# Kernel optimization log

Hardware: AMD Instinct MI355X
Metric: run time of the kernel (lower is better)

The kernel has to match this reference:

```python
import jax, jax.numpy as jnp
import numpy as np

# Master-Slave MoE: dense shared 'master' expert Mlp applied to every token,
# plus num_experts 'slave' Mlp experts combined via top-k softmax gating,
# output = master(x) + sum_k gate_k * expert_k(x). Each Mlp: fc2(gelu(fc1(x))).

DIM = 512
HID = 4 * DIM
NUM_EXPERTS = 8
TOP_K = 2


def mlp(x, w1, b1, w2, b2):
    h = jax.nn.gelu(jnp.einsum('bnd,dh->bnh', x, w1) + b1)
    return jnp.einsum('bnh,hd->bnd', h, w2) + b2


def setup_inputs() -> dict:
    key = jax.random.key(0)
    ks = jax.random.split(key, 10)
    B, N = 4, 4096
    s1 = 1.0 / np.sqrt(DIM)
    s2 = 1.0 / np.sqrt(HID)
    return {
        'x': jax.random.normal(ks[0], (B, N, DIM), jnp.float32),
        'gate_w': jax.random.normal(ks[1], (DIM, NUM_EXPERTS), jnp.float32) * s1,
        'master_w1': jax.random.normal(ks[2], (DIM, HID), jnp.float32) * s1,
        'master_b1': jnp.zeros((HID,), jnp.float32),
        'master_w2': jax.random.normal(ks[3], (HID, DIM), jnp.float32) * s2,
        'master_b2': jnp.zeros((DIM,), jnp.float32),
        'expert_w1': jax.random.normal(ks[4], (NUM_EXPERTS, DIM, HID), jnp.float32) * s1,
        'expert_b1': jnp.zeros((NUM_EXPERTS, HID), jnp.float32),
        'expert_w2': jax.random.normal(ks[5], (NUM_EXPERTS, HID, DIM), jnp.float32) * s2,
        'expert_b2': jnp.zeros((NUM_EXPERTS, DIM), jnp.float32),
    }


def reference(x, gate_w, master_w1, master_b1, master_w2, master_b2,
              expert_w1, expert_b1, expert_w2, expert_b2):
    B, N, D = x.shape
    # Router: top-k softmax gating over experts
    logits = jnp.einsum('bnd,de->bne', x, gate_w)  # [B,N,E]
    topv, topi = jax.lax.top_k(logits, TOP_K)       # [B,N,K]
    gates_k = jax.nn.softmax(topv, axis=-1)         # [B,N,K]
    # dense gate matrix [B,N,E] (zeros for non-selected experts)
    gates = jnp.zeros_like(logits)
    gates = jnp.take_along_axis(gates, topi, axis=-1)  # noop to keep shape clarity
    gates = jnp.zeros_like(logits).at[
        jnp.arange(B)[:, None, None],
        jnp.arange(N)[None, :, None],
        topi].set(gates_k)

    # Master (shared) expert applied to all tokens
    master_out = mlp(x, master_w1, master_b1, master_w2, master_b2)

    # Slave experts: compute per-expert Mlp (vectorized over experts),
    # combine with gate weights. Gate is sparse (only top-k nonzero),
    # mathematically equal to token routing.
    h = jax.nn.gelu(jnp.einsum('bnd,edh->ebnh', x, expert_w1)
                    + expert_b1[:, None, None, :])          # [E,B,N,H]
    eo = jnp.einsum('ebnh,ehd->ebnd', h, expert_w2) \
         + expert_b2[:, None, None, :]                       # [E,B,N,D]
    slave_out = jnp.einsum('bne,ebnd->bnd', gates, eo)

    return master_out + slave_out
```

## Files before the change

### kernel.cpp

```cpp
#include <hip/hip_runtime.h>

#define DIM 512
#define HID 2048
#define NE 8

typedef _Float16 half8v __attribute__((ext_vector_type(8)));
typedef _Float16 half4v __attribute__((ext_vector_type(4)));
typedef float f32x4 __attribute__((ext_vector_type(4)));

__device__ __forceinline__ void gload16(const void* g, void* l) {
  __builtin_amdgcn_global_load_lds(
      (const __attribute__((address_space(1))) void*)g,
      (__attribute__((address_space(3))) void*)l, 16, 0, 0);
}

__global__ void k_transpose_cast9(const float* __restrict__ src_e,
                                  const float* __restrict__ src_m,
                                  _Float16* __restrict__ dst, int R, int C) {
  __shared__ _Float16 ts[64][66];
  int z = blockIdx.z;
  const float* src = (z == NE) ? src_m : src_e + (size_t)z * R * C;
  _Float16* d = dst + (size_t)z * R * C;
  int c0 = blockIdx.x * 64, r0 = blockIdx.y * 64;
  int t = threadIdx.x;
  int rr = t >> 4, cc = (t & 15) * 4;
  #pragma unroll
  for (int i = 0; i < 4; i++) {
    int row = rr + i * 16;
    float4 v = *(const float4*)&src[(size_t)(r0 + row) * C + c0 + cc];
    ts[row][cc + 0] = (_Float16)v.x; ts[row][cc + 1] = (_Float16)v.y;
    ts[row][cc + 2] = (_Float16)v.z; ts[row][cc + 3] = (_Float16)v.w;
  }
  __syncthreads();
  int cr = t >> 4, rb = (t & 15) * 4;
  #pragma unroll
  for (int i = 0; i < 4; i++) {
    int c = cr + i * 16;
    half4v o = { ts[rb + 0][c], ts[rb + 1][c], ts[rb + 2][c], ts[rb + 3][c] };
    *(half4v*)&d[(size_t)(c0 + c) * R + r0 + rb] = o;
  }
}

#define RT_TOK 16
__global__ void k_router(const float* __restrict__ x, const float* __restrict__ gw,
                         _Float16* __restrict__ xb,
                         int* __restrict__ counts, int* __restrict__ perm,
                         float* __restrict__ pgate, int T) {
  __shared__ float xs[RT_TOK][520];
  __shared__ float gwt[8][520];
  __shared__ float lg[RT_TOK][8];
  int t = threadIdx.x;
  int tk0 = blockIdx.x * RT_TOK;
  for (int i = t; i < DIM * NE; i += 128) {
    int k = i >> 3, e = i & 7;
    gwt[e][k] = gw[i];
  }
  for (int i = t; i < RT_TOK * (DIM / 4); i += 128) {
    int row = i >> 7; int c4 = i & 127;
    float4 v = *(const float4*)&x[(size_t)(tk0 + row) * DIM + c4 * 4];
    xs[row][c4 * 4 + 0] = v.x; xs[row][c4 * 4 + 1] = v.y;
    xs[row][c4 * 4 + 2] = v.z; xs[row][c4 * 4 + 3] = v.w;
    half4v h = { (_Float16)v.x, (_Float16)v.y, (_Float16)v.z, (_Float16)v.w };
    *(half4v*)&xb[(size_t)(tk0 + row) * DIM + c4 * 4] = h;
  }
  __syncthreads();
  int tok = t >> 3, e = t & 7;
  float acc = 0.f;
  for (int k = 0; k < DIM; k += 4) {
    float4 xv = *(const float4*)&xs[tok][k];
    float4 wv = *(const float4*)&gwt[e][k];
    acc += xv.x * wv.x + xv.y * wv.y + xv.z * wv.z + xv.w * wv.w;
  }
  lg[tok][e] = acc;
  __syncthreads();
  if (t < RT_TOK) {
    float v0 = -1e30f, v1 = -1e30f; int i0 = 0, i1 = 0;
    #pragma unroll
    for (int j = 0; j < 8; j++) { float v = lg[t][j]; if (v > v0) { v0 = v; i0 = j; } }
    #pragma unroll
    for (int j = 0; j < 8; j++) { if (j == i0) continue; float v = lg[t][j]; if (v > v1) { v1 = v; i1 = j; } }
    float g0 = 1.f / (1.f + __expf(v1 - v0));
    float g1 = 1.f - g0;
    int token = tk0 + t;
    int p0 = atomicAdd(&counts[i0], 1);
    perm[i0 * T + p0] = token; pgate[i0 * T + p0] = g0;
    int p1 = atomicAdd(&counts[i1], 1);
    perm[i1 * T + p1] = token; pgate[i1 * T + p1] = g1;
  }
}


template<int K, int MODE>
__global__ __launch_bounds__(512, 1) void k_gemm(
    const _Float16* __restrict__ A,
    const _Float16* __restrict__ Bt,
    const float* __restrict__ ebias,
    const float* __restrict__ mbias,
    const int* __restrict__ counts,
    const int* __restrict__ perm,
    const float* __restrict__ pgate,
    _Float16* __restrict__ hout,
    float* __restrict__ out,
    int T) {
  constexpr int N = (MODE == 0) ? HID : DIM;
  constexpr int KT = K / 64;
  extern __shared__ char S[];
  int e = blockIdx.z;
  bool isM = (e == NE);
  int count = isM ? T : counts[e];
  int m0 = blockIdx.x * 256;
  if (m0 >= count) return;
  int n0 = blockIdx.y * 256;
  int hbase = 0;
  if (isM) hbase = 2 * T;
  else for (int i = 0; i < e; i++) hbase += counts[i];
  const _Float16* Be = Bt + (size_t)e * N * K;
  const float* be = isM ? mbias : ebias + (size_t)e * N;

  int t = threadIdx.x;
  int lane = t & 63;
  int wid = t >> 6;
  int wm = (wid >> 2) * 128;
  int wn = (wid & 3) * 64;

  int srow = t >> 3;
  int schunk = (t & 7) ^ (srow & 7);
  const char *aP0, *aP1, *aP2, *aP3, *bP0, *bP1, *bP2, *bP3;
  {
    int r0 = srow, r1 = 64 + srow, r2 = 128 + srow, r3 = 192 + srow;
    int p0 = m0 + r0; p0 = p0 < count ? p0 : count - 1;
    int p1 = m0 + r1; p1 = p1 < count ? p1 : count - 1;
    int p2 = m0 + r2; p2 = p2 < count ? p2 : count - 1;
    int p3 = m0 + r3; p3 = p3 < count ? p3 : count - 1;
    int a0, a1, a2, a3;
    if (MODE == 0) {
      a0 = isM ? p0 : perm[e * T + p0];
      a1 = isM ? p1 : perm[e * T + p1];
      a2 = isM ? p2 : perm[e * T + p2];
      a3 = isM ? p3 : perm[e * T + p3];
    } else {
      a0 = hbase + p0; a1 = hbase + p1; a2 = hbase + p2; a3 = hbase + p3;
    }
    aP0 = (const char*)(A + (size_t)a0 * K) + schunk * 16;
    aP1 = (const char*)(A + (size_t)a1 * K) + schunk * 16;
    aP2 = (const char*)(A + (size_t)a2 * K) + schunk * 16;
    aP3 = (const char*)(A + (size_t)a3 * K) + schunk * 16;
    bP0 = (const char*)(Be + (size_t)(n0 + r0) * K) + schunk * 16;
    bP1 = (const char*)(Be + (size_t)(n0 + r1) * K) + schunk * 16;
    bP2 = (const char*)(Be + (size_t)(n0 + r2) * K) + schunk * 16;
    bP3 = (const char*)(Be + (size_t)(n0 + r3) * K) + schunk * 16;
  }

  int l15 = lane & 15, l4 = lane >> 4, l7 = lane & 7;
  int roff0 = l15 * 128 + ((l4 ^ l7) << 4);
  int roff1 = l15 * 128 + (((4 + l4) ^ l7) << 4);

  f32x4 acc[8][4] = {};

  char* buf0 = S;
  char* buf1 = S + 65536;

#define STAGE(base, ktile) do { \
    const int off_ = (ktile) * 128; \
    gload16(aP0 + off_, (base) + t * 16); \
    gload16(aP1 + off_, (base) + 8192 + t * 16); \
    gload16(aP2 + off_, (base) + 16384 + t * 16); \
    gload16(aP3 + off_, (base) + 24576 + t * 16); \
    gload16(bP0 + off_, (base) + 32768 + t * 16); \
    gload16(bP1 + off_, (base) + 40960 + t * 16); \
    gload16(bP2 + off_, (base) + 49152 + t * 16); \
    gload16(bP3 + off_, (base) + 57344 + t * 16); \
  } while (0)

  STAGE(buf0, 0);
  for (int kt = 0; kt < KT; ++kt) {
    __builtin_amdgcn_s_barrier();
    if (kt + 1 < KT) {
      STAGE((kt & 1) ? buf0 : buf1, kt + 1);
      asm volatile("s_waitcnt vmcnt(8)" ::: "memory");
    } else {
      asm volatile("s_waitcnt vmcnt(0)" ::: "memory");
    }
    __builtin_amdgcn_sched_barrier(0);
    __builtin_amdgcn_s_barrier();
    const char* base = (kt & 1) ? buf1 : buf0;
    const char* ab = base;
    const char* bb = base + 32768;
    __builtin_amdgcn_s_setprio(1);
    #pragma unroll
    for (int kk = 0; kk < 2; ++kk) {
      int ro = kk ? roff1 : roff0;
      half8v af[8], bf[4];
      #pragma unroll
      for (int mi = 0; mi < 8; mi++)
        af[mi] = *(const half8v*)(ab + (wm + mi * 16) * 128 + ro);
      #pragma unroll
      for (int ni = 0; ni < 4; ni++)
        bf[ni] = *(const half8v*)(bb + (wn + ni * 16) * 128 + ro);
      #pragma unroll
      for (int mi = 0; mi < 8; mi++)
        #pragma unroll
        for (int ni = 0; ni < 4; ni++)
          acc[mi][ni] = __builtin_amdgcn_mfma_f32_16x16x32_f16(af[mi], bf[ni], acc[mi][ni], 0, 0, 0);
    }
    __builtin_amdgcn_s_setprio(0);
  }
#undef STAGE

  int cl = l15, rh = l4 * 4;
  float bv[4];
  #pragma unroll
  for (int ni = 0; ni < 4; ni++) bv[ni] = be[n0 + wn + ni * 16 + cl];
  #pragma unroll
  for (int mi = 0; mi < 8; mi++) {
    #pragma unroll
    for (int r = 0; r < 4; r++) {
      int pos = m0 + wm + mi * 16 + rh + r;
      if (pos >= count) continue;
      int orow; float g = 1.f;
      if (MODE == 0) orow = hbase + pos;
      else {
        orow = isM ? pos : perm[e * T + pos];
        if (!isM) g = pgate[e * T + pos];
      }
      #pragma unroll
      for (int ni = 0; ni < 4; ni++) {
        float v = acc[mi][ni][r] + bv[ni];
        int col = n0 + wn + ni * 16 + cl;
        if (MODE == 0) {
          float ge = v / (1.f + __expf(-1.5957691216057308f * (v + 0.044715f * v * v * v)));
          hout[(size_t)orow * HID + col] = (_Float16)ge;
        } else {
          unsafeAtomicAdd(&out[(size_t)orow * DIM + col], g * v);
        }
      }
    }
  }
}

extern "C" void kernel_launch(void* const* d_in, const int* in_sizes, int n_in,
                              void* d_out, int out_size, void* d_ws, size_t ws_size,
                              hipStream_t stream) {
  const float* x         = (const float*)d_in[0];
  const float* gate_w    = (const float*)d_in[1];
  const float* master_w1 = (const float*)d_in[2];
  const float* master_b1 = (const float*)d_in[3];
  const float* master_w2 = (const float*)d_in[4];
  const float* master_b2 = (const float*)d_in[5];
  const float* expert_w1 = (const float*)d_in[6];
  const float* expert_b1 = (const float*)d_in[7];
  const float* expert_w2 = (const float*)d_in[8];
  const float* expert_b2 = (const float*)d_in[9];
  float* out = (float*)d_out;
  int T = in_sizes[0] / DIM;

  char* p = (char*)d_ws;
  _Float16* xb   = (_Float16*)p; p += (size_t)T * DIM * 2;
  _Float16* wb1t = (_Float16*)p; p += (size_t)9 * HID * DIM * 2;
  _Float16* wb2t = (_Float16*)p; p += (size_t)9 * DIM * HID * 2;
  int*   counts  = (int*)p;      p += 256;
  int*   perm    = (int*)p;      p += (size_t)8 * T * 4;
  float* pgate   = (float*)p;    p += (size_t)8 * T * 4;
  _Float16* hbuf = (_Float16*)p; p += (size_t)3 * T * HID * 2;

  (void)hipFuncSetAttribute((const void*)&k_gemm<DIM, 0>,
                            hipFuncAttributeMaxDynamicSharedMemorySize, 131072);
  (void)hipFuncSetAttribute((const void*)&k_gemm<HID, 2>,
                            hipFuncAttributeMaxDynamicSharedMemorySize, 131072);

  hipMemsetAsync(counts, 0, 64, stream);
  hipMemsetAsync(out, 0, (size_t)T * DIM * 4, stream);

  k_router<<<T / RT_TOK, 128, 0, stream>>>(x, gate_w, xb, counts, perm, pgate, T);

  k_transpose_cast9<<<dim3(HID / 64, DIM / 64, 9), 256, 0, stream>>>(
      expert_w1, master_w1, wb1t, DIM, HID);
  k_transpose_cast9<<<dim3(DIM / 64, HID / 64, 9), 256, 0, stream>>>(
      expert_w2, master_w2, wb2t, HID, DIM);

  k_gemm<DIM, 0><<<dim3(T / 256, HID / 256, 9), 512, 131072, stream>>>(
      xb, wb1t, expert_b1, master_b1, counts, perm, nullptr,
      hbuf, nullptr, T);
  k_gemm<HID, 2><<<dim3(T / 256, DIM / 256, 9), 512, 131072, stream>>>(
      hbuf, wb2t, expert_b2, master_b2, counts, perm, pgate,
      nullptr, out, T);
}
```

Baseline: 717.3 us.

## Pack expert segments into a compact 1D grid and split master down-projection out

```diff
diff --git a/kernel.cpp b/kernel.cpp
--- a/kernel.cpp
+++ b/kernel.cpp
@@ -101,21 +101,43 @@
     const float* __restrict__ pgate,
     _Float16* __restrict__ hout,
     float* __restrict__ out,
-    int T) {
+    int T, int gxd8) {
   constexpr int N = (MODE == 0) ? HID : DIM;
   constexpr int KT = K / 64;
   extern __shared__ char S[];
-  int e = blockIdx.z;
-  bool isM = (e == NE);
-  int count = isM ? T : counts[e];
-  int m0 = blockIdx.x * 256;
-  if (m0 >= count) return;
+
+  int bxi = blockIdx.x;
+  bxi = (bxi & 7) * gxd8 + (bxi >> 3);
+  int bx = bxi * 256;
+  int e = 8, segbase = 0, count;
+  if (MODE == 1) {
+    #pragma unroll
+    for (int i = 0; i < 8; i++) segbase += (counts[i] + 255) & ~255;
+    count = T;
+  } else {
+    #pragma unroll
+    for (int i = 0; i < 8; i++) {
+      int seglen = (counts[i] + 255) & ~255;
+      if (e == 8 && bx < segbase + seglen) { e = i; break; }
+      segbase += seglen;
+    }
+    if (e == 8) {
+      if (MODE == 2) return;
+      count = T;
+      if (bx - segbase >= T) return;
+    } else {
+      count = counts[e];
+    }
+  }
+  bool isM = (e == 8);
+  int m0 = (MODE == 1) ? bx : bx - segbase;
+  if (MODE == 1 && m0 >= T) return;
   int n0 = blockIdx.y * 256;
-  int hbase = 0;
-  if (isM) hbase = 2 * T;
-  else for (int i = 0; i < e; i++) hbase += counts[i];
-  const _Float16* Be = Bt + (size_t)e * N * K;
-  const float* be = isM ? mbias : ebias + (size_t)e * N;
+  const _Float16* Be = Bt + (size_t)(MODE == 1 ? 8 : e) * N * K;
+  const float* be;
+  if (MODE == 0) be = isM ? mbias : ebias + (size_t)e * N;
+  else if (MODE == 1) be = mbias;
+  else be = ebias + (size_t)e * N;
 
   int t = threadIdx.x;
   int lane = t & 63;
@@ -139,7 +161,7 @@
       a2 = isM ? p2 : perm[e * T + p2];
       a3 = isM ? p3 : perm[e * T + p3];
     } else {
-      a0 = hbase + p0; a1 = hbase + p1; a2 = hbase + p2; a3 = hbase + p3;
+      a0 = segbase + p0; a1 = segbase + p1; a2 = segbase + p2; a3 = segbase + p3;
     }
     aP0 = (const char*)(A + (size_t)a0 * K) + schunk * 16;
     aP1 = (const char*)(A + (size_t)a1 * K) + schunk * 16;
@@ -218,10 +240,11 @@
       int pos = m0 + wm + mi * 16 + rh + r;
       if (pos >= count) continue;
       int orow; float g = 1.f;
-      if (MODE == 0) orow = hbase + pos;
+      if (MODE == 0) orow = segbase + pos;
+      else if (MODE == 1) orow = pos;
       else {
-        orow = isM ? pos : perm[e * T + pos];
-        if (!isM) g = pgate[e * T + pos];
+        orow = perm[e * T + pos];
+        g = pgate[e * T + pos];
       }
       #pragma unroll
       for (int ni = 0; ni < 4; ni++) {
@@ -230,6 +253,8 @@
         if (MODE == 0) {
           float ge = v / (1.f + __expf(-1.5957691216057308f * (v + 0.044715f * v * v * v)));
           hout[(size_t)orow * HID + col] = (_Float16)ge;
+        } else if (MODE == 1) {
+          out[(size_t)orow * DIM + col] = v;
         } else {
           unsafeAtomicAdd(&out[(size_t)orow * DIM + col], g * v);
         }
@@ -261,15 +286,16 @@
   int*   counts  = (int*)p;      p += 256;
   int*   perm    = (int*)p;      p += (size_t)8 * T * 4;
   float* pgate   = (float*)p;    p += (size_t)8 * T * 4;
-  _Float16* hbuf = (_Float16*)p; p += (size_t)3 * T * HID * 2;
+  _Float16* hbuf = (_Float16*)p; p += (size_t)(3 * T + 2048) * HID * 2;
 
   (void)hipFuncSetAttribute((const void*)&k_gemm<DIM, 0>,
+                            hipFuncAttributeMaxDynamicSharedMemorySize, 131072);
+  (void)hipFuncSetAttribute((const void*)&k_gemm<HID, 1>,
                             hipFuncAttributeMaxDynamicSharedMemorySize, 131072);
   (void)hipFuncSetAttribute((const void*)&k_gemm<HID, 2>,
                             hipFuncAttributeMaxDynamicSharedMemorySize, 131072);
 
   hipMemsetAsync(counts, 0, 64, stream);
-  hipMemsetAsync(out, 0, (size_t)T * DIM * 4, stream);
 
   k_router<<<T / RT_TOK, 128, 0, stream>>>(x, gate_w, xb, counts, perm, pgate, T);
 
@@ -278,10 +304,18 @@
   k_transpose_cast9<<<dim3(DIM / 64, HID / 64, 9), 256, 0, stream>>>(
       expert_w2, master_w2, wb2t, HID, DIM);
 
-  k_gemm<DIM, 0><<<dim3(T / 256, HID / 256, 9), 512, 131072, stream>>>(
+  int gx1 = 3 * T / 256 + 8;
+  k_gemm<DIM, 0><<<dim3(gx1, HID / 256, 1), 512, 131072, stream>>>(
       xb, wb1t, expert_b1, master_b1, counts, perm, nullptr,
-      hbuf, nullptr, T);
-  k_gemm<HID, 2><<<dim3(T / 256, DIM / 256, 9), 512, 131072, stream>>>(
+      hbuf, nullptr, T, gx1 / 8);
+
+  int gxm = T / 256;
+  k_gemm<HID, 1><<<dim3(gxm, DIM / 256, 1), 512, 131072, stream>>>(
+      hbuf, wb2t, expert_b2, master_b2, counts, perm, nullptr,
+      nullptr, out, T, gxm / 8);
+
+  int gxe = 2 * T / 256 + 8;
+  k_gemm<HID, 2><<<dim3(gxe, DIM / 256, 1), 512, 131072, stream>>>(
       hbuf, wb2t, expert_b2, master_b2, counts, perm, pgate,
-      nullptr, out, T);
-}
+      nullptr, out, T, gxe / 8);
+}
```

Measured after the change: 609.8 us. 1.18x faster.
